# Performance work log

Measured on AMD Instinct MI355X. Metric: run time of the kernel, lower is better.

Reference implementation:

```python
import jax, jax.numpy as jnp
import numpy as np
from jax import lax

B, CIN, COUT, H, W = 8, 64, 64, 128, 128
KH = KW = 3
STRIDE = PAD = DIL = 1
DG = 1
BOUND = 8.0
HOUT = (H + 2 * PAD - (DIL * (KH - 1) + 1)) // STRIDE + 1
WOUT = (W + 2 * PAD - (DIL * (KW - 1) + 1)) // STRIDE + 1
K = KH * KW


def setup_inputs() -> dict:
    key = jax.random.key(0)
    k0, k1, k2, k3 = jax.random.split(key, 4)
    x = jax.random.normal(k0, (B, CIN, H, W), dtype=jnp.float32)
    weight = jax.random.normal(k1, (COUT, CIN, KH, KW), dtype=jnp.float32) * 0.05
    # conv_offset params (zero-init in the original; randomized here to exercise sampling)
    off_w = jax.random.normal(k2, (2 * K * DG, CIN, 3, 3), dtype=jnp.float32) * 0.01
    off_b = jax.random.normal(k3, (2 * K * DG,), dtype=jnp.float32) * 0.1
    return {"x": x, "weight": weight, "off_w": off_w, "off_b": off_b}


def _conv_offset(x, off_w, off_b):
    # 3x3 conv, stride 1, pad 1 -> [B, 2*K*DG, H, W]
    o = lax.conv_general_dilated(x, off_w, (1, 1), [(1, 1), (1, 1)],
                                 dimension_numbers=("NCHW", "OIHW", "NCHW"))
    return o + off_b[None, :, None, None]


def _deform_conv(x, offset, weight):
    Bn, C, Hin, Win = x.shape
    # offset channel layout: per tap k, channel 2k = y-offset, 2k+1 = x-offset (dg=1)
    off = offset.reshape(Bn, K, 2, HOUT, WOUT)
    off_y, off_x = off[:, :, 0], off[:, :, 1]          # [B, K, Ho, Wo]
    tap_y = jnp.repeat(jnp.arange(KH) * DIL, KW).astype(jnp.float32)  # [K]
    tap_x = jnp.tile(jnp.arange(KW) * DIL, KH).astype(jnp.float32)    # [K]
    base_y = (jnp.arange(HOUT) * STRIDE - PAD).astype(jnp.float32)    # [Ho]
    base_x = (jnp.arange(WOUT) * STRIDE - PAD).astype(jnp.float32)    # [Wo]
    sy = off_y + tap_y[None, :, None, None] + base_y[None, None, :, None]  # [B,K,Ho,Wo]
    sx = off_x + tap_x[None, :, None, None] + base_x[None, None, None, :]

    y0f = jnp.floor(sy)
    x0f = jnp.floor(sx)
    ty = sy - y0f
    tx = sx - x0f
    y0 = y0f.astype(jnp.int32)
    x0 = x0f.astype(jnp.int32)

    img = x.reshape(Bn, C, Hin * Win)
    gather = jax.vmap(lambda im, ix: im[:, ix])  # ([C,HW],[K,Ho,Wo]) -> [C,K,Ho,Wo]

    acc = jnp.zeros((Bn, C, K, HOUT, WOUT), dtype=x.dtype)
    for dy in (0, 1):
        for dx in (0, 1):
            yc = y0 + dy
            xc = x0 + dx
            wgt = (ty if dy else 1.0 - ty) * (tx if dx else 1.0 - tx)
            valid = ((yc >= 0) & (yc < Hin) & (xc >= 0) & (xc < Win)).astype(x.dtype)
            idx = jnp.clip(yc, 0, Hin - 1) * Win + jnp.clip(xc, 0, Win - 1)
            acc = acc + (wgt * valid)[:, None] * gather(img, idx)

    # groups == 1: plain weighted accumulate over taps and input channels
    return jnp.einsum("bckhw,ock->bohw", acc, weight.reshape(COUT, CIN, K))


def reference(x, weight, off_w, off_b):
    offset = jnp.clip(_conv_offset(x, off_w, off_b), -BOUND, BOUND)
    return _deform_conv(x, offset, weight)
```

## Files before the change

kernel.cpp:

```cpp
#include <hip/hip_runtime.h>
#include <math.h>

typedef float  f32x4  __attribute__((ext_vector_type(4)));
typedef __bf16 bf16x8 __attribute__((ext_vector_type(8)));

#define B_  8
#define C_  64
#define O_  64
#define H_  128
#define W_  128
#define K_  9
#define OFFC_ 18
#define HW_ (H_*W_)

#define SWZ(row, cb) ((row)*128 + ((cb) ^ (((row)&7)<<4)))

#define XTB_BYTES  16777216
#define OFFS_BYTES 9437184
#define WTB_BYTES  73728

__global__ __launch_bounds__(256) void k_transpose(const float* __restrict__ x,
                                                   __bf16* __restrict__ xtb) {
    __shared__ float tile[64][65];
    int gid = blockIdx.x;
    int w0 = (gid & 1) * 64;
    int h  = (gid >> 1) & 127;
    int b  = gid >> 8;
    int tid = threadIdx.x;

    int lw = tid & 63, cq = tid >> 6;
    const float* xb = x + ((size_t)b * C_) * HW_ + (size_t)h * W_;
    #pragma unroll
    for (int it = 0; it < 16; ++it) {
        int c = it * 4 + cq;
        tile[c][lw] = xb[(size_t)c * HW_ + w0 + lw];
    }
    __syncthreads();
    int p = tid >> 2, q = tid & 3;
    bf16x8 v0, v1;
    #pragma unroll
    for (int j = 0; j < 8; ++j) {
        v0[j] = (__bf16)tile[q * 16 + j][p];
        v1[j] = (__bf16)tile[q * 16 + 8 + j][p];
    }
    __bf16* dst = xtb + (((size_t)b * H_ + h) * W_ + w0 + p) * C_ + q * 16;
    *(bf16x8*)dst = v0;
    *(bf16x8*)(dst + 8) = v1;
}

__global__ __launch_bounds__(256) void k_wtrans(const float* __restrict__ w,
                                                const float* __restrict__ ow,
                                                __bf16* __restrict__ wtb,
                                                __bf16* __restrict__ owt) {
    int i = blockIdx.x * 256 + threadIdx.x;
    if (i < 9 * 64 * 64) {
        int c = i & 63, o = (i >> 6) & 63, k = i >> 12;
        wtb[i] = (__bf16)w[(o * 64 + c) * 9 + k];
    }
    if (i < 9 * 32 * 64) {
        int c = i & 63, o = (i >> 6) & 31, k = i >> 11;
        owt[i] = (o < OFFC_) ? (__bf16)ow[(o * 64 + c) * 9 + k] : (__bf16)0.f;
    }
}

__global__ __launch_bounds__(256) void k_offconv(const __bf16* __restrict__ xtb,
                                                 const __bf16* __restrict__ owt,
                                                 const float* __restrict__ off_b,
                                                 float* __restrict__ offs) {
    __shared__ alignas(16) short wlo[9 * 32 * 64];
    char* wb = (char*)wlo;
    int gid = blockIdx.x, tid = threadIdx.x;
    int w0 = (gid & 1) * 64, h = (gid >> 1) & 127, b = gid >> 8;

    const bf16x8* wsrc = (const bf16x8*)owt;
    for (int q = tid; q < 9 * 32 * 8; q += 256) {
        int tap = q >> 8, o = (q >> 3) & 31, cb = (q & 7) * 16;
        *(bf16x8*)(wb + tap * 4096 + SWZ(o, cb)) = wsrc[q];
    }

    int lane = tid & 63, wv = tid >> 6;
    int l15 = lane & 15, lg = lane >> 4;

    f32x4 acc[2];
    #pragma unroll
    for (int mi = 0; mi < 2; ++mi)
        #pragma unroll
        for (int r = 0; r < 4; ++r) {
            int o = mi * 16 + lg * 4 + r;
            acc[mi][r] = (o < OFFC_) ? off_b[o] : 0.f;
        }
    __syncthreads();

    int px = wv * 16 + l15;
    #pragma unroll
    for (int tap = 0; tap < 9; ++tap) {
        int y  = h + tap / 3 - 1;
        int xw = w0 + px + tap % 3 - 1;
        bool valid = ((unsigned)y < 128u) && ((unsigned)xw < 128u);
        const __bf16* bsrc = xtb + (((size_t)b * H_ + y) * W_ + xw) * C_ + lg * 8;
        #pragma unroll
        for (int ks = 0; ks < 2; ++ks) {
            int cb = ks * 64 + lg * 16;
            bf16x8 a0 = *(const bf16x8*)(wb + tap * 4096 + SWZ(l15, cb));
            bf16x8 a1 = *(const bf16x8*)(wb + tap * 4096 + SWZ(16 + l15, cb));
            bf16x8 bv;
            #pragma unroll
            for (int j = 0; j < 8; ++j) bv[j] = (__bf16)0.f;
            if (valid) bv = *(const bf16x8*)(bsrc + ks * 32);
            acc[0] = __builtin_amdgcn_mfma_f32_16x16x32_bf16(a0, bv, acc[0], 0, 0, 0);
            acc[1] = __builtin_amdgcn_mfma_f32_16x16x32_bf16(a1, bv, acc[1], 0, 0, 0);
        }
    }

    float* obase = offs + (((size_t)b * H_ + h) * W_ + w0 + px) * OFFC_;
    #pragma unroll
    for (int mi = 0; mi < 2; ++mi)
        #pragma unroll
        for (int r = 0; r < 4; ++r) {
            int o = mi * 16 + lg * 4 + r;
            if (o < OFFC_) obase[o] = fminf(8.f, fmaxf(-8.f, acc[mi][r]));
        }
}

__global__ __launch_bounds__(256) void k_deform(const __bf16* __restrict__ xtb,
                                                const float* __restrict__ offs,
                                                const __bf16* __restrict__ wtb,
                                                float* __restrict__ out) {
    __shared__ alignas(16) short wl[64 * 64];
    __shared__ alignas(16) short sm[64 * 64];
    __shared__ float offl[64][18];
    char* wlb = (char*)wl;
    char* spb = (char*)sm;

    int gid = blockIdx.x, tid = threadIdx.x;
    int w0 = (gid & 1) * 64, h = (gid >> 1) & 127, b = gid >> 8;

    const float* osrc = offs + (((size_t)b * H_ + h) * W_ + w0) * OFFC_;
    for (int i = tid; i < 64 * OFFC_; i += 256) ((float*)offl)[i] = osrc[i];

    int p = tid >> 2, cq = tid & 3;
    int lane = tid & 63, wv = tid >> 6;
    int l15 = lane & 15, lg = lane >> 4;
    int m2 = (wv >> 1) * 2, n2 = (wv & 1) * 2;

    f32x4 acc[2][2];
    #pragma unroll
    for (int mi = 0; mi < 2; ++mi)
        #pragma unroll
        for (int ni = 0; ni < 2; ++ni)
            #pragma unroll
            for (int r = 0; r < 4; ++r) acc[mi][ni][r] = 0.f;

    const __bf16* xb = xtb + (size_t)b * HW_ * C_;
    float fh = (float)(h - 1);
    float fw = (float)(w0 + p - 1);

    #pragma unroll 1
    for (int k = 0; k < 9; ++k) {
        __syncthreads();
        const bf16x8* wsrc = (const bf16x8*)(wtb + (size_t)k * 4096);
        #pragma unroll
        for (int t = 0; t < 2; ++t) {
            int qq = tid + t * 256;
            int o = qq >> 3, cb = (qq & 7) * 16;
            *(bf16x8*)(wlb + SWZ(o, cb)) = wsrc[qq];
        }
        {
            float2 o2 = *(const float2*)&offl[p][2 * k];
            float sy = o2.x + (float)(k / 3) + fh;
            float sx = o2.y + (float)(k % 3) + fw;
            float y0f = floorf(sy), x0f = floorf(sx);
            float ty = sy - y0f, tx = sx - x0f;
            int y0 = (int)y0f, x0 = (int)x0f;
            float r[16];
            #pragma unroll
            for (int j = 0; j < 16; ++j) r[j] = 0.f;
            #pragma unroll
            for (int dy = 0; dy < 2; ++dy) {
                int yc = y0 + dy;
                if ((unsigned)yc < 128u) {
                    float wy = dy ? ty : 1.f - ty;
                    #pragma unroll
                    for (int dx = 0; dx < 2; ++dx) {
                        int xc = x0 + dx;
                        if ((unsigned)xc < 128u) {
                            float wgt = wy * (dx ? tx : 1.f - tx);
                            const bf16x8* src = (const bf16x8*)(xb + ((size_t)yc * W_ + xc) * C_ + cq * 16);
                            bf16x8 v0 = src[0], v1 = src[1];
                            #pragma unroll
                            for (int j = 0; j < 8; ++j) {
                                r[j]     += wgt * (float)v0[j];
                                r[8 + j] += wgt * (float)v1[j];
                            }
                        }
                    }
                }
            }
            bf16x8 h0, h1;
            #pragma unroll
            for (int j = 0; j < 8; ++j) { h0[j] = (__bf16)r[j]; h1[j] = (__bf16)r[8 + j]; }
            int cb0 = cq * 32;
            *(bf16x8*)(spb + SWZ(p, cb0))      = h0;
            *(bf16x8*)(spb + SWZ(p, cb0 + 16)) = h1;
        }
        __syncthreads();
        #pragma unroll
        for (int ks = 0; ks < 2; ++ks) {
            int cb = ks * 64 + lg * 16;
            bf16x8 afr[2], bfr[2];
            #pragma unroll
            for (int mi = 0; mi < 2; ++mi) {
                int o = (m2 + mi) * 16 + l15;
                afr[mi] = *(const bf16x8*)(wlb + SWZ(o, cb));
            }
            #pragma unroll
            for (int ni = 0; ni < 2; ++ni) {
                int px = (n2 + ni) * 16 + l15;
                bfr[ni] = *(const bf16x8*)(spb + SWZ(px, cb));
            }
            #pragma unroll
            for (int mi = 0; mi < 2; ++mi)
                #pragma unroll
                for (int ni = 0; ni < 2; ++ni)
                    acc[mi][ni] = __builtin_amdgcn_mfma_f32_16x16x32_bf16(afr[mi], bfr[ni], acc[mi][ni], 0, 0, 0);
        }
    }

    #pragma unroll
    for (int mi = 0; mi < 2; ++mi)
        #pragma unroll
        for (int ni = 0; ni < 2; ++ni)
            #pragma unroll
            for (int rr = 0; rr < 4; ++rr) {
                int o  = (m2 + mi) * 16 + lg * 4 + rr;
                int px = (n2 + ni) * 16 + l15;
                out[((size_t)b * O_ + o) * HW_ + h * W_ + w0 + px] = acc[mi][ni][rr];
            }
}

extern "C" void kernel_launch(void* const* d_in, const int* in_sizes, int n_in,
                              void* d_out, int out_size, void* d_ws, size_t ws_size,
                              hipStream_t stream) {
    const float* x      = (const float*)d_in[0];
    const float* weight = (const float*)d_in[1];
    const float* off_w  = (const float*)d_in[2];
    const float* off_b  = (const float*)d_in[3];
    float* out = (float*)d_out;

    char* ws = (char*)d_ws;
    __bf16* xtb = (__bf16*)ws;
    float*  offs = (float*)(ws + XTB_BYTES);
    __bf16* wtb = (__bf16*)(ws + XTB_BYTES + OFFS_BYTES);
    __bf16* owt = (__bf16*)(ws + XTB_BYTES + OFFS_BYTES + WTB_BYTES);

    k_transpose<<<2048, 256, 0, stream>>>(x, xtb);
    k_wtrans<<<144, 256, 0, stream>>>(weight, off_w, wtb, owt);
    k_offconv<<<2048, 256, 0, stream>>>(xtb, owt, off_b, offs);
    k_deform<<<2048, 256, 0, stream>>>(xtb, offs, wtb, out);
}
```

Baseline: 91.88 us.

## Pad input with zero halo, fuse prep kernels, software-pipeline deform gather and weight loads

Transposes x into a zero-padded 160x160 NHWC bf16 buffer so the offset conv and the bilinear gather can drop their bounds checks, and merges the transpose, padding and weight-transpose steps into a single prep kernel. Weights are pre-swizzled and copied straight into LDS with global_load_lds. The deform kernel now prefetches corner samples and weights for the next taps into triple- and double-buffered LDS and registers, leaving one barrier per tap. The pipelining uses more registers and LDS, and the halo is only 16 pixels wide, so it holds only while offsets stay within the ±8 clip.

```diff
diff --git a/kernel.cpp b/kernel.cpp
--- a/kernel.cpp
+++ b/kernel.cpp
@@ -4,238 +4,267 @@
 typedef float  f32x4  __attribute__((ext_vector_type(4)));
 typedef __bf16 bf16x8 __attribute__((ext_vector_type(8)));
 
-#define B_  8
-#define C_  64
-#define O_  64
-#define H_  128
-#define W_  128
-#define K_  9
-#define OFFC_ 18
-#define HW_ (H_*W_)
+#define HP_     160
+#define PITCH_  (HP_*64)
+#define BPITCH_ (HP_*HP_*64)
 
 #define SWZ(row, cb) ((row)*128 + ((cb) ^ (((row)&7)<<4)))
 
-#define XTB_BYTES  16777216
+#define XP_BYTES   26214400
 #define OFFS_BYTES 9437184
 #define WTB_BYTES  73728
 
-__global__ __launch_bounds__(256) void k_transpose(const float* __restrict__ x,
-                                                   __bf16* __restrict__ xtb) {
-    __shared__ float tile[64][65];
-    int gid = blockIdx.x;
-    int w0 = (gid & 1) * 64;
-    int h  = (gid >> 1) & 127;
-    int b  = gid >> 8;
-    int tid = threadIdx.x;
-
-    int lw = tid & 63, cq = tid >> 6;
-    const float* xb = x + ((size_t)b * C_) * HW_ + (size_t)h * W_;
-    #pragma unroll
-    for (int it = 0; it < 16; ++it) {
-        int c = it * 4 + cq;
-        tile[c][lw] = xb[(size_t)c * HW_ + w0 + lw];
-    }
-    __syncthreads();
-    int p = tid >> 2, q = tid & 3;
-    bf16x8 v0, v1;
-    #pragma unroll
-    for (int j = 0; j < 8; ++j) {
-        v0[j] = (__bf16)tile[q * 16 + j][p];
-        v1[j] = (__bf16)tile[q * 16 + 8 + j][p];
-    }
-    __bf16* dst = xtb + (((size_t)b * H_ + h) * W_ + w0 + p) * C_ + q * 16;
-    *(bf16x8*)dst = v0;
-    *(bf16x8*)(dst + 8) = v1;
-}
-
-__global__ __launch_bounds__(256) void k_wtrans(const float* __restrict__ w,
-                                                const float* __restrict__ ow,
-                                                __bf16* __restrict__ wtb,
-                                                __bf16* __restrict__ owt) {
-    int i = blockIdx.x * 256 + threadIdx.x;
-    if (i < 9 * 64 * 64) {
-        int c = i & 63, o = (i >> 6) & 63, k = i >> 12;
-        wtb[i] = (__bf16)w[(o * 64 + c) * 9 + k];
-    }
-    if (i < 9 * 32 * 64) {
-        int c = i & 63, o = (i >> 6) & 31, k = i >> 11;
-        owt[i] = (o < OFFC_) ? (__bf16)ow[(o * 64 + c) * 9 + k] : (__bf16)0.f;
-    }
-}
-
-__global__ __launch_bounds__(256) void k_offconv(const __bf16* __restrict__ xtb,
+__device__ __forceinline__ void gl_lds16(const void* g, void* l) {
+    __builtin_amdgcn_global_load_lds(
+        (const __attribute__((address_space(1))) void*)g,
+        (__attribute__((address_space(3))) void*)l, 16, 0, 0);
+}
+
+__global__ __launch_bounds__(256) void k_prep(const float* __restrict__ x,
+                                              const float* __restrict__ w,
+                                              const float* __restrict__ ow,
+                                              __bf16* __restrict__ xp,
+                                              __bf16* __restrict__ wtb,
+                                              __bf16* __restrict__ owt) {
+    int gid = blockIdx.x, tid = threadIdx.x;
+    if (gid < 2048) {
+        __shared__ float tile[64][65];
+        int w0 = (gid & 1) * 64, h = (gid >> 1) & 127, b = gid >> 8;
+        int lw = tid & 63, cq4 = tid >> 6;
+        const float* xb = x + ((size_t)b * 64) * 16384 + (size_t)h * 128;
+        #pragma unroll
+        for (int it = 0; it < 16; ++it) {
+            int c = it * 4 + cq4;
+            tile[c][lw] = xb[(size_t)c * 16384 + w0 + lw];
+        }
+        __syncthreads();
+        int p = tid >> 2, q = tid & 3;
+        bf16x8 v0, v1;
+        #pragma unroll
+        for (int j = 0; j < 8; ++j) {
+            v0[j] = (__bf16)tile[q * 16 + j][p];
+            v1[j] = (__bf16)tile[q * 16 + 8 + j][p];
+        }
+        __bf16* dst = xp + (size_t)b * BPITCH_ + (size_t)(h + 16) * PITCH_
+                         + (size_t)(w0 + p + 16) * 64 + q * 16;
+        *(bf16x8*)dst = v0;
+        *(bf16x8*)(dst + 8) = v1;
+    } else if (gid < 4352) {
+        int i = (gid - 2048) * 256 + tid;
+        int b, y, xc, cc;
+        if (i < 327680) {
+            b = i / 40960; int r = i % 40960;
+            int row = r / 1280; y = row < 16 ? row : row + 128;
+            int xi = r % 1280; xc = xi >> 3; cc = (xi & 7) * 8;
+        } else {
+            int j = i - 327680;
+            b = j / 32768; int r = j % 32768;
+            y = 16 + (r >> 8);
+            int xi = r & 255; int xcol = xi >> 3;
+            xc = xcol < 16 ? xcol : xcol + 128; cc = (xi & 7) * 8;
+        }
+        bf16x8 z;
+        #pragma unroll
+        for (int j = 0; j < 8; ++j) z[j] = (__bf16)0.f;
+        *(bf16x8*)(xp + (size_t)b * BPITCH_ + (size_t)y * PITCH_ + (size_t)xc * 64 + cc) = z;
+    } else {
+        int i = (gid - 4352) * 256 + tid;
+        if (i < 36864) {
+            int c = i & 63, o = (i >> 6) & 63, k = i >> 12;
+            wtb[(k << 12) + (o << 6) + (c ^ ((o & 7) << 3))] = (__bf16)w[(o * 64 + c) * 9 + k];
+        }
+        if (i < 18432) {
+            int c = i & 63, o = (i >> 6) & 31, k = i >> 11;
+            owt[(k << 11) + (o << 6) + (c ^ ((o & 7) << 3))] =
+                (o < 18) ? (__bf16)ow[(o * 64 + c) * 9 + k] : (__bf16)0.f;
+        }
+    }
+}
+
+__global__ __launch_bounds__(256) void k_offconv(const __bf16* __restrict__ xp,
                                                  const __bf16* __restrict__ owt,
                                                  const float* __restrict__ off_b,
                                                  float* __restrict__ offs) {
     __shared__ alignas(16) short wlo[9 * 32 * 64];
-    char* wb = (char*)wlo;
     int gid = blockIdx.x, tid = threadIdx.x;
     int w0 = (gid & 1) * 64, h = (gid >> 1) & 127, b = gid >> 8;
-
-    const bf16x8* wsrc = (const bf16x8*)owt;
-    for (int q = tid; q < 9 * 32 * 8; q += 256) {
-        int tap = q >> 8, o = (q >> 3) & 31, cb = (q & 7) * 16;
-        *(bf16x8*)(wb + tap * 4096 + SWZ(o, cb)) = wsrc[q];
-    }
-
-    int lane = tid & 63, wv = tid >> 6;
-    int l15 = lane & 15, lg = lane >> 4;
-
-    f32x4 acc[2];
-    #pragma unroll
-    for (int mi = 0; mi < 2; ++mi)
-        #pragma unroll
-        for (int r = 0; r < 4; ++r) {
-            int o = mi * 16 + lg * 4 + r;
-            acc[mi][r] = (o < OFFC_) ? off_b[o] : 0.f;
-        }
+    int lane = tid & 63, wv = tid >> 6, l15 = lane & 15, lg = lane >> 4;
+
+    {
+        const char* s = (const char*)owt + wv * 9216 + lane * 16;
+        char* d = (char*)wlo + wv * 9216;
+        #pragma unroll
+        for (int it = 0; it < 9; ++it) gl_lds16(s + it * 1024, d + it * 1024);
+    }
+
+    f32x4 acc0, acc1;
+    #pragma unroll
+    for (int r = 0; r < 4; ++r) {
+        int o = lg * 4 + r;
+        acc0[r] = (o < 18) ? off_b[o] : 0.f;
+        acc1[r] = (o + 16 < 18) ? off_b[o + 16] : 0.f;
+    }
     __syncthreads();
 
     int px = wv * 16 + l15;
+    const __bf16* pbase = xp + (size_t)b * BPITCH_ + (size_t)(h + 15) * PITCH_
+                             + (size_t)(w0 + px + 15) * 64 + lg * 8;
     #pragma unroll
     for (int tap = 0; tap < 9; ++tap) {
-        int y  = h + tap / 3 - 1;
-        int xw = w0 + px + tap % 3 - 1;
-        bool valid = ((unsigned)y < 128u) && ((unsigned)xw < 128u);
-        const __bf16* bsrc = xtb + (((size_t)b * H_ + y) * W_ + xw) * C_ + lg * 8;
+        const __bf16* bsrc = pbase + (tap / 3) * PITCH_ + (tap % 3) * 64;
+        const char* wb = (const char*)wlo + tap * 4096;
         #pragma unroll
         for (int ks = 0; ks < 2; ++ks) {
             int cb = ks * 64 + lg * 16;
-            bf16x8 a0 = *(const bf16x8*)(wb + tap * 4096 + SWZ(l15, cb));
-            bf16x8 a1 = *(const bf16x8*)(wb + tap * 4096 + SWZ(16 + l15, cb));
-            bf16x8 bv;
-            #pragma unroll
-            for (int j = 0; j < 8; ++j) bv[j] = (__bf16)0.f;
-            if (valid) bv = *(const bf16x8*)(bsrc + ks * 32);
-            acc[0] = __builtin_amdgcn_mfma_f32_16x16x32_bf16(a0, bv, acc[0], 0, 0, 0);
-            acc[1] = __builtin_amdgcn_mfma_f32_16x16x32_bf16(a1, bv, acc[1], 0, 0, 0);
-        }
-    }
-
-    float* obase = offs + (((size_t)b * H_ + h) * W_ + w0 + px) * OFFC_;
-    #pragma unroll
-    for (int mi = 0; mi < 2; ++mi)
-        #pragma unroll
-        for (int r = 0; r < 4; ++r) {
-            int o = mi * 16 + lg * 4 + r;
-            if (o < OFFC_) obase[o] = fminf(8.f, fmaxf(-8.f, acc[mi][r]));
-        }
-}
-
-__global__ __launch_bounds__(256) void k_deform(const __bf16* __restrict__ xtb,
+            bf16x8 a0 = *(const bf16x8*)(wb + SWZ(l15, cb));
+            bf16x8 a1 = *(const bf16x8*)(wb + SWZ(16 + l15, cb));
+            bf16x8 bv = *(const bf16x8*)(bsrc + ks * 32);
+            acc0 = __builtin_amdgcn_mfma_f32_16x16x32_bf16(a0, bv, acc0, 0, 0, 0);
+            acc1 = __builtin_amdgcn_mfma_f32_16x16x32_bf16(a1, bv, acc1, 0, 0, 0);
+        }
+    }
+    float* obase = offs + (((size_t)b * 128 + h) * 128 + w0 + px) * 18;
+    #pragma unroll
+    for (int r = 0; r < 4; ++r) {
+        int o = lg * 4 + r;
+        if (o < 18) obase[o] = fminf(8.f, fmaxf(-8.f, acc0[r]));
+        if (o + 16 < 18) obase[o + 16] = fminf(8.f, fmaxf(-8.f, acc1[r]));
+    }
+}
+
+struct CBank {
+    bf16x8 v00a, v00b, v01a, v01b, v10a, v10b, v11a, v11b;
+    float ty, tx;
+};
+
+__device__ __forceinline__ void load_corners(int tap, CBank& bk,
+                                             const float (*offl)[18], int p,
+                                             float fh, float fwp,
+                                             const __bf16* xb) {
+    float2 od = *(const float2*)&offl[p][2 * tap];
+    float sy = od.x + (float)(tap / 3) + fh;
+    float sx = od.y + (float)(tap % 3) + fwp;
+    float yf = floorf(sy), xf = floorf(sx);
+    bk.ty = sy - yf; bk.tx = sx - xf;
+    int yi = (int)yf, xi = (int)xf;
+    const __bf16* s0 = xb + (size_t)(yi * HP_ + xi) * 64;
+    bk.v00a = ((const bf16x8*)s0)[0];        bk.v00b = ((const bf16x8*)s0)[1];
+    bk.v01a = ((const bf16x8*)(s0 + 64))[0]; bk.v01b = ((const bf16x8*)(s0 + 64))[1];
+    const __bf16* s1 = s0 + PITCH_;
+    bk.v10a = ((const bf16x8*)s1)[0];        bk.v10b = ((const bf16x8*)s1)[1];
+    bk.v11a = ((const bf16x8*)(s1 + 64))[0]; bk.v11b = ((const bf16x8*)(s1 + 64))[1];
+}
+
+__device__ __forceinline__ void interp_store(const CBank& bk, char* smb,
+                                             int p, int cq) {
+    float ty = bk.ty, tx = bk.tx;
+    float w00 = (1.f - ty) * (1.f - tx), w01 = (1.f - ty) * tx;
+    float w10 = ty * (1.f - tx),         w11 = ty * tx;
+    bf16x8 h0, h1;
+    #pragma unroll
+    for (int j = 0; j < 8; ++j) {
+        float r0 = w00 * (float)bk.v00a[j] + w01 * (float)bk.v01a[j]
+                 + w10 * (float)bk.v10a[j] + w11 * (float)bk.v11a[j];
+        float r1 = w00 * (float)bk.v00b[j] + w01 * (float)bk.v01b[j]
+                 + w10 * (float)bk.v10b[j] + w11 * (float)bk.v11b[j];
+        h0[j] = (__bf16)r0; h1[j] = (__bf16)r1;
+    }
+    int cb0 = cq * 32;
+    *(bf16x8*)(smb + SWZ(p, cb0))      = h0;
+    *(bf16x8*)(smb + SWZ(p, cb0 + 16)) = h1;
+}
+
+__global__ __launch_bounds__(256) void k_deform(const __bf16* __restrict__ xp,
                                                 const float* __restrict__ offs,
                                                 const __bf16* __restrict__ wtb,
                                                 float* __restrict__ out) {
-    __shared__ alignas(16) short wl[64 * 64];
-    __shared__ alignas(16) short sm[64 * 64];
+    __shared__ alignas(16) short wl[3][4096];
+    __shared__ alignas(16) short sm[2][4096];
     __shared__ float offl[64][18];
-    char* wlb = (char*)wl;
-    char* spb = (char*)sm;
 
     int gid = blockIdx.x, tid = threadIdx.x;
     int w0 = (gid & 1) * 64, h = (gid >> 1) & 127, b = gid >> 8;
-
-    const float* osrc = offs + (((size_t)b * H_ + h) * W_ + w0) * OFFC_;
-    for (int i = tid; i < 64 * OFFC_; i += 256) ((float*)offl)[i] = osrc[i];
-
+    int lane = tid & 63, wv = tid >> 6, l15 = lane & 15, lg = lane >> 4;
     int p = tid >> 2, cq = tid & 3;
-    int lane = tid & 63, wv = tid >> 6;
-    int l15 = lane & 15, lg = lane >> 4;
     int m2 = (wv >> 1) * 2, n2 = (wv & 1) * 2;
 
-    f32x4 acc[2][2];
-    #pragma unroll
-    for (int mi = 0; mi < 2; ++mi)
-        #pragma unroll
-        for (int ni = 0; ni < 2; ++ni)
-            #pragma unroll
-            for (int r = 0; r < 4; ++r) acc[mi][ni][r] = 0.f;
-
-    const __bf16* xb = xtb + (size_t)b * HW_ * C_;
-    float fh = (float)(h - 1);
-    float fw = (float)(w0 + p - 1);
-
-    #pragma unroll 1
+    const char* wsrc = (const char*)wtb;
+    {
+        const char* s = wsrc + wv * 2048 + lane * 16;
+        char* d = (char*)wl[0] + wv * 2048;
+        gl_lds16(s, d); gl_lds16(s + 1024, d + 1024);
+    }
+    {
+        const float* osrc = offs + (((size_t)b * 128 + h) * 128 + w0) * 18;
+        float* od = &offl[0][0];
+        #pragma unroll
+        for (int it = 0; it < 5; ++it) {
+            int i = tid + it * 256;
+            if (i < 1152) od[i] = osrc[i];
+        }
+    }
+    __syncthreads();
+
+    const __bf16* xb = xp + (size_t)b * BPITCH_ + cq * 16;
+    float fh  = (float)(h - 1 + 16);
+    float fwp = (float)(w0 + p - 1 + 16);
+
+    CBank bk0, bk1;
+    load_corners(0, bk0, offl, p, fh, fwp, xb);
+    {
+        const char* s = wsrc + 8192 + wv * 2048 + lane * 16;
+        char* d = (char*)wl[1] + wv * 2048;
+        gl_lds16(s, d); gl_lds16(s + 1024, d + 1024);
+    }
+    interp_store(bk0, (char*)sm[0], p, cq);
+    load_corners(1, bk1, offl, p, fh, fwp, xb);
+    __syncthreads();
+
+    f32x4 acc00, acc01, acc10, acc11;
+    #pragma unroll
+    for (int r = 0; r < 4; ++r) { acc00[r] = 0.f; acc01[r] = 0.f; acc10[r] = 0.f; acc11[r] = 0.f; }
+
+    #pragma unroll
     for (int k = 0; k < 9; ++k) {
-        __syncthreads();
-        const bf16x8* wsrc = (const bf16x8*)(wtb + (size_t)k * 4096);
-        #pragma unroll
-        for (int t = 0; t < 2; ++t) {
-            int qq = tid + t * 256;
-            int o = qq >> 3, cb = (qq & 7) * 16;
-            *(bf16x8*)(wlb + SWZ(o, cb)) = wsrc[qq];
-        }
-        {
-            float2 o2 = *(const float2*)&offl[p][2 * k];
-            float sy = o2.x + (float)(k / 3) + fh;
-            float sx = o2.y + (float)(k % 3) + fw;
-            float y0f = floorf(sy), x0f = floorf(sx);
-            float ty = sy - y0f, tx = sx - x0f;
-            int y0 = (int)y0f, x0 = (int)x0f;
-            float r[16];
-            #pragma unroll
-            for (int j = 0; j < 16; ++j) r[j] = 0.f;
-            #pragma unroll
-            for (int dy = 0; dy < 2; ++dy) {
-                int yc = y0 + dy;
-                if ((unsigned)yc < 128u) {
-                    float wy = dy ? ty : 1.f - ty;
-                    #pragma unroll
-                    for (int dx = 0; dx < 2; ++dx) {
-                        int xc = x0 + dx;
-                        if ((unsigned)xc < 128u) {
-                            float wgt = wy * (dx ? tx : 1.f - tx);
-                            const bf16x8* src = (const bf16x8*)(xb + ((size_t)yc * W_ + xc) * C_ + cq * 16);
-                            bf16x8 v0 = src[0], v1 = src[1];
-                            #pragma unroll
-                            for (int j = 0; j < 8; ++j) {
-                                r[j]     += wgt * (float)v0[j];
-                                r[8 + j] += wgt * (float)v1[j];
-                            }
-                        }
-                    }
-                }
-            }
-            bf16x8 h0, h1;
-            #pragma unroll
-            for (int j = 0; j < 8; ++j) { h0[j] = (__bf16)r[j]; h1[j] = (__bf16)r[8 + j]; }
-            int cb0 = cq * 32;
-            *(bf16x8*)(spb + SWZ(p, cb0))      = h0;
-            *(bf16x8*)(spb + SWZ(p, cb0 + 16)) = h1;
-        }
-        __syncthreads();
+        const char* wb = (const char*)wl[k % 3];
+        const char* sb = (const char*)sm[k & 1];
         #pragma unroll
         for (int ks = 0; ks < 2; ++ks) {
             int cb = ks * 64 + lg * 16;
-            bf16x8 afr[2], bfr[2];
+            bf16x8 aA = *(const bf16x8*)(wb + SWZ(m2 * 16 + l15, cb));
+            bf16x8 aB = *(const bf16x8*)(wb + SWZ((m2 + 1) * 16 + l15, cb));
+            bf16x8 bA = *(const bf16x8*)(sb + SWZ(n2 * 16 + l15, cb));
+            bf16x8 bB = *(const bf16x8*)(sb + SWZ((n2 + 1) * 16 + l15, cb));
+            acc00 = __builtin_amdgcn_mfma_f32_16x16x32_bf16(aA, bA, acc00, 0, 0, 0);
+            acc01 = __builtin_amdgcn_mfma_f32_16x16x32_bf16(aA, bB, acc01, 0, 0, 0);
+            acc10 = __builtin_amdgcn_mfma_f32_16x16x32_bf16(aB, bA, acc10, 0, 0, 0);
+            acc11 = __builtin_amdgcn_mfma_f32_16x16x32_bf16(aB, bB, acc11, 0, 0, 0);
+        }
+        if (k < 7) {
+            load_corners(k + 2, (k & 1) ? bk1 : bk0, offl, p, fh, fwp, xb);
+            const char* s = wsrc + (k + 2) * 8192 + wv * 2048 + lane * 16;
+            char* d = (char*)wl[(k + 2) % 3] + wv * 2048;
+            gl_lds16(s, d); gl_lds16(s + 1024, d + 1024);
+        }
+        if (k < 8) {
+            interp_store((k & 1) ? bk0 : bk1, (char*)sm[(k + 1) & 1], p, cq);
+            __syncthreads();
+        }
+    }
+
+    #pragma unroll
+    for (int mi = 0; mi < 2; ++mi)
+        #pragma unroll
+        for (int ni = 0; ni < 2; ++ni) {
+            f32x4 a = (mi == 0) ? (ni == 0 ? acc00 : acc01)
+                                : (ni == 0 ? acc10 : acc11);
             #pragma unroll
-            for (int mi = 0; mi < 2; ++mi) {
-                int o = (m2 + mi) * 16 + l15;
-                afr[mi] = *(const bf16x8*)(wlb + SWZ(o, cb));
+            for (int r = 0; r < 4; ++r) {
+                int o  = (m2 + mi) * 16 + lg * 4 + r;
+                int px = (n2 + ni) * 16 + l15;
+                out[((size_t)b * 64 + o) * 16384 + (size_t)h * 128 + w0 + px] = a[r];
             }
-            #pragma unroll
-            for (int ni = 0; ni < 2; ++ni) {
-                int px = (n2 + ni) * 16 + l15;
-                bfr[ni] = *(const bf16x8*)(spb + SWZ(px, cb));
-            }
-            #pragma unroll
-            for (int mi = 0; mi < 2; ++mi)
-                #pragma unroll
-                for (int ni = 0; ni < 2; ++ni)
-                    acc[mi][ni] = __builtin_amdgcn_mfma_f32_16x16x32_bf16(afr[mi], bfr[ni], acc[mi][ni], 0, 0, 0);
-        }
-    }
-
-    #pragma unroll
-    for (int mi = 0; mi < 2; ++mi)
-        #pragma unroll
-        for (int ni = 0; ni < 2; ++ni)
-            #pragma unroll
-            for (int rr = 0; rr < 4; ++rr) {
-                int o  = (m2 + mi) * 16 + lg * 4 + rr;
-                int px = (n2 + ni) * 16 + l15;
-                out[((size_t)b * O_ + o) * HW_ + h * W_ + w0 + px] = acc[mi][ni][rr];
-            }
+        }
 }
 
 extern "C" void kernel_launch(void* const* d_in, const int* in_sizes, int n_in,
@@ -248,13 +277,12 @@
     float* out = (float*)d_out;
 
     char* ws = (char*)d_ws;
-    __bf16* xtb = (__bf16*)ws;
-    float*  offs = (float*)(ws + XTB_BYTES);
-    __bf16* wtb = (__bf16*)(ws + XTB_BYTES + OFFS_BYTES);
-    __bf16* owt = (__bf16*)(ws + XTB_BYTES + OFFS_BYTES + WTB_BYTES);
-
-    k_transpose<<<2048, 256, 0, stream>>>(x, xtb);
-    k_wtrans<<<144, 256, 0, stream>>>(weight, off_w, wtb, owt);
-    k_offconv<<<2048, 256, 0, stream>>>(xtb, owt, off_b, offs);
-    k_deform<<<2048, 256, 0, stream>>>(xtb, offs, wtb, out);
-}
+    __bf16* xp  = (__bf16*)ws;
+    float*  offs = (float*)(ws + XP_BYTES);
+    __bf16* wtb = (__bf16*)(ws + XP_BYTES + OFFS_BYTES);
+    __bf16* owt = (__bf16*)(ws + XP_BYTES + OFFS_BYTES + WTB_BYTES);
+
+    k_prep<<<4496, 256, 0, stream>>>(x, weight, off_w, xp, wtb, owt);
+    k_offconv<<<2048, 256, 0, stream>>>(xp, owt, off_b, offs);
+    k_deform<<<2048, 256, 0, stream>>>(xp, offs, wtb, out);
+}
```

After: 78.40 us. 14.7% less time.
